# Kernel tuning notes

Measured on AMD Instinct MI355X. Metric: run time of the kernel, lower is better.

## Reference

```python
import jax, jax.numpy as jnp
import numpy as np

N, E = 10000, 160000
F_IN, H1, C1, C2 = 256, 8, 128, 128
SLOPE = 0.2  # PyG GATConv default negative_slope


def setup_inputs() -> dict:
    key = jax.random.key(0)
    ks = jax.random.split(key, 9)
    s = 0.05
    return {
        "x": jax.random.normal(ks[0], (N, F_IN), jnp.float32),
        "edge_index": jax.random.randint(ks[1], (2, E), 0, N),
        "W1": jax.random.normal(ks[2], (F_IN, H1 * C1), jnp.float32) * s,
        "a_src1": jax.random.normal(ks[3], (H1, C1), jnp.float32) * s,
        "a_dst1": jax.random.normal(ks[4], (H1, C1), jnp.float32) * s,
        "b1": jnp.zeros((H1 * C1,), jnp.float32),
        "W2": jax.random.normal(ks[5], (H1 * C1, C2), jnp.float32) * s,
        "a_src2": jax.random.normal(ks[6], (1, C2), jnp.float32) * s,
        "a_dst2": jax.random.normal(ks[7], (1, C2), jnp.float32) * s,
        "b2": jnp.zeros((C2,), jnp.float32),
    }


def gat_conv(x, src, dst, W, a_s, a_d, b, heads, out_ch, concat):
    n = x.shape[0]
    h = (x @ W).reshape(n, heads, out_ch)            # [N,H,C]
    s_src = jnp.einsum("nhc,hc->nh", h, a_s)         # [N,H]
    s_dst = jnp.einsum("nhc,hc->nh", h, a_d)
    e = jax.nn.leaky_relu(s_src[src] + s_dst[dst], SLOPE)   # [Etot,H]
    # segment softmax over incoming edges per destination (self-loops guarantee non-empty segments)
    m = jax.lax.stop_gradient(jax.ops.segment_max(e, dst, num_segments=n))
    p = jnp.exp(e - m[dst])
    denom = jax.ops.segment_sum(p, dst, num_segments=n)
    alpha = p / denom[dst]                            # [Etot,H]
    out = jax.ops.segment_sum(h[src] * alpha[:, :, None], dst, num_segments=n)  # [N,H,C]
    out = out.reshape(n, heads * out_ch) if concat else out.mean(axis=1)
    return out + b


def reference(x, edge_index, W1, a_src1, a_dst1, b1, W2, a_src2, a_dst2, b2):
    n = x.shape[0]
    loops = jnp.arange(n, dtype=edge_index.dtype)     # PyG add_self_loops=True
    src = jnp.concatenate([edge_index[0], loops])
    dst = jnp.concatenate([edge_index[1], loops])
    # dropout layers are identity at inference (training=False)
    h1 = jax.nn.elu(gat_conv(x, src, dst, W1, a_src1, a_dst1, b1, H1, C1, True))
    return gat_conv(h1, src, dst, W2, a_src2, a_dst2, b2, 1, C2, False)
```

## Files before the change

kernel.cpp:

```cpp
#include <hip/hip_runtime.h>
#include <math.h>

#define F_IN 256
#define H1 8
#define C1 128
#define HC1 1024
#define C2 128
#define SLOPE 0.2f

typedef unsigned short u16;
typedef __attribute__((ext_vector_type(8))) short bf16x8;
typedef __attribute__((ext_vector_type(4))) float f32x4;


__device__ __forceinline__ float lrelu(float v) { return v > 0.f ? v : SLOPE * v; }

__device__ __forceinline__ unsigned bf16_rne(float x) {
    unsigned u = __float_as_uint(x);
    u += 0x7fffu + ((u >> 16) & 1u);
    return u >> 16;
}

__device__ __forceinline__ void split2(float a, float b, unsigned& hi, unsigned& lo) {
    unsigned ha = bf16_rne(a), hb = bf16_rne(b);
    float fa = __uint_as_float(ha << 16), fb = __uint_as_float(hb << 16);
    hi = ha | (hb << 16);
    lo = bf16_rne(a - fa) | (bf16_rne(b - fb) << 16);
}

__device__ __forceinline__ void gload16(const u16* g, u16* l) {
    __builtin_amdgcn_global_load_lds(
        (const __attribute__((address_space(1))) unsigned*)g,
        (__attribute__((address_space(3))) unsigned*)l, 16, 0, 0);
}


__global__ void init_deg(int* deg, int n) {
    int i = blockIdx.x * blockDim.x + threadIdx.x;
    if (i < n) deg[i] = 1;
}

__global__ void hist_kernel(const int* __restrict__ dst, int* __restrict__ deg, int E) {
    int i = blockIdx.x * blockDim.x + threadIdx.x;
    if (i < E) atomicAdd(&deg[dst[i]], 1);
}

__global__ void scan_kernel(const int* __restrict__ deg, int* __restrict__ start,
                            int* __restrict__ cursor, int n) {
    __shared__ int buf[1024];
    int carry = 0;
    for (int base = 0; base < n; base += 1024) {
        int i = base + (int)threadIdx.x;
        int v = (i < n) ? deg[i] : 0;
        buf[threadIdx.x] = v;
        __syncthreads();
        for (int offd = 1; offd < 1024; offd <<= 1) {
            int tv = 0;
            if ((int)threadIdx.x >= offd) tv = buf[threadIdx.x - offd];
            __syncthreads();
            if ((int)threadIdx.x >= offd) buf[threadIdx.x] += tv;
            __syncthreads();
        }
        int incl = buf[threadIdx.x];
        if (i < n) { start[i] = carry + incl - v; cursor[i] = carry + incl - v; }
        carry += buf[1023];
        __syncthreads();
    }
    if (threadIdx.x == 0) start[n] = carry;
}

__global__ void scatter_kernel(const int* __restrict__ src, const int* __restrict__ dst,
                               int* __restrict__ cursor, int* __restrict__ ssorted,
                               unsigned char* __restrict__ rowloc,
                               int E, int N) {
    int i = blockIdx.x * blockDim.x + threadIdx.x;
    if (i < E) {
        int d = dst[i];
        int pos = atomicAdd(&cursor[d], 1);
        ssorted[pos] = src[i];
        rowloc[pos] = (unsigned char)(d & 15);
    } else if (i < E + N) {
        int d = i - E;
        int pos = atomicAdd(&cursor[d], 1);
        ssorted[pos] = d;
        rowloc[pos] = (unsigned char)(d & 15);
    }
}


__global__ void split_mat(const float* __restrict__ in, u16* __restrict__ hi,
                          u16* __restrict__ lo, int n) {
    int i = blockIdx.x * blockDim.x + threadIdx.x;
    if (i >= n) return;
    float v = in[i];
    unsigned h = bf16_rne(v);
    hi[i] = (u16)h;
    lo[i] = (u16)bf16_rne(v - __uint_as_float(h << 16));
}

__global__ void split_transpose(const float* __restrict__ in, u16* __restrict__ hi,
                                u16* __restrict__ lo, int R, int C) {
    int i = blockIdx.x * blockDim.x + threadIdx.x;
    if (i >= R * C) return;
    int r = i / C, c = i % C;
    float v = in[i];
    unsigned h = bf16_rne(v);
    hi[(size_t)c * R + r] = (u16)h;
    lo[(size_t)c * R + r] = (u16)bf16_rne(v - __uint_as_float(h << 16));
}


__global__ __launch_bounds__(256) void gemm_mfma(const u16* __restrict__ Ahi,
                                                 const u16* __restrict__ Alo,
                                                 const u16* __restrict__ Bhi,
                                                 const u16* __restrict__ Blo,
                                                 u16* __restrict__ Cbf,
                                                 int M, int N, int K) {
    __shared__ u16 lds[16384];
    const int t = threadIdx.x;
    const int rbase = blockIdx.y * 128;
    const int cbase = blockIdx.x * 128;

    const int lane = t & 63;
    const int R0 = (t >> 7) << 6;
    const int C0 = ((t >> 6) & 1) << 6;
    const int lrow = lane & 15;
    const int kq = lane >> 4;

    f32x4 acc[4][4] = {};

    for (int k0 = 0; k0 < K; k0 += 32) {
#pragma unroll
        for (int i = 0; i < 2; i++) {
            int c = t + (i << 8);
            int row = c >> 2;
            int kc = (c & 3) << 3;
            int ar = min(rbase + row, M - 1);
            int br = cbase + row;
            gload16(Ahi + (size_t)ar * K + k0 + kc, &lds[c * 8]);
            gload16(Alo + (size_t)ar * K + k0 + kc, &lds[4096 + c * 8]);
            gload16(Bhi + (size_t)br * K + k0 + kc, &lds[8192 + c * 8]);
            gload16(Blo + (size_t)br * K + k0 + kc, &lds[12288 + c * 8]);
        }
        __syncthreads();

        bf16x8 ah[4], al[4], bh[4], bl[4];
#pragma unroll
        for (int m = 0; m < 4; m++) {
            int off = (R0 + (m << 4) + lrow) * 32 + (kq << 3);
            ah[m] = *(const bf16x8*)&lds[off];
            al[m] = *(const bf16x8*)&lds[4096 + off];
        }
#pragma unroll
        for (int n = 0; n < 4; n++) {
            int off = (C0 + (n << 4) + lrow) * 32 + (kq << 3);
            bh[n] = *(const bf16x8*)&lds[8192 + off];
            bl[n] = *(const bf16x8*)&lds[12288 + off];
        }
#pragma unroll
        for (int m = 0; m < 4; m++)
#pragma unroll
            for (int n = 0; n < 4; n++) {
                acc[m][n] = __builtin_amdgcn_mfma_f32_16x16x32_bf16(ah[m], bh[n], acc[m][n], 0, 0, 0);
                acc[m][n] = __builtin_amdgcn_mfma_f32_16x16x32_bf16(ah[m], bl[n], acc[m][n], 0, 0, 0);
                acc[m][n] = __builtin_amdgcn_mfma_f32_16x16x32_bf16(al[m], bh[n], acc[m][n], 0, 0, 0);
            }
        __syncthreads();
    }

#pragma unroll
    for (int m = 0; m < 4; m++)
#pragma unroll
        for (int n = 0; n < 4; n++) {
            int col = cbase + C0 + (n << 4) + lrow;
#pragma unroll
            for (int r = 0; r < 4; r++) {
                int row = rbase + R0 + (m << 4) + kq * 4 + r;
                if (row < M) Cbf[(size_t)row * N + col] = (u16)bf16_rne(acc[m][n][r]);
            }
        }
}


__global__ __launch_bounds__(256) void gemm_mfma64(const u16* __restrict__ Ahi,
                                                   const u16* __restrict__ Alo,
                                                   const u16* __restrict__ Bhi,
                                                   const u16* __restrict__ Blo,
                                                   u16* __restrict__ Cbf,
                                                   int M, int N, int K) {
    __shared__ u16 lds[16384];
    const int t = threadIdx.x;
    const int rbase = blockIdx.y * 64;
    const int cbase = blockIdx.x * 64;

    const int lane = t & 63;
    const int w = t >> 6;
    const int R0 = (w >> 1) << 5;
    const int C0 = (w & 1) << 5;
    const int lrow = lane & 15;
    const int kq = lane >> 4;

    f32x4 acc[2][2] = {};

    for (int k0 = 0; k0 < K; k0 += 64) {
        {
            int row = (w << 4) + (lane >> 2);
            int kcc = (lane & 3) << 3;
            int ar = min(rbase + row, M - 1);
            int br = cbase + row;
            const size_t ga = (size_t)ar * K + k0 + kcc;
            const size_t gb = (size_t)br * K + k0 + kcc;
            const int ldo = row * 32 + kcc;
#pragma unroll
            for (int s2 = 0; s2 < 2; s2++) {
                gload16(Ahi + ga + s2 * 32, &lds[s2 * 2048 + ldo]);
                gload16(Alo + ga + s2 * 32, &lds[4096 + s2 * 2048 + ldo]);
                gload16(Bhi + gb + s2 * 32, &lds[8192 + s2 * 2048 + ldo]);
                gload16(Blo + gb + s2 * 32, &lds[12288 + s2 * 2048 + ldo]);
            }
        }
        __syncthreads();

#pragma unroll
        for (int s = 0; s < 2; s++) {
            bf16x8 ah[2], al[2], bh[2], bl[2];
#pragma unroll
            for (int m = 0; m < 2; m++) {
                int off = s * 2048 + (R0 + (m << 4) + lrow) * 32 + (kq << 3);
                ah[m] = *(const bf16x8*)&lds[off];
                al[m] = *(const bf16x8*)&lds[4096 + off];
            }
#pragma unroll
            for (int n = 0; n < 2; n++) {
                int off = s * 2048 + (C0 + (n << 4) + lrow) * 32 + (kq << 3);
                bh[n] = *(const bf16x8*)&lds[8192 + off];
                bl[n] = *(const bf16x8*)&lds[12288 + off];
            }
#pragma unroll
            for (int m = 0; m < 2; m++)
#pragma unroll
                for (int n = 0; n < 2; n++) {
                    acc[m][n] = __builtin_amdgcn_mfma_f32_16x16x32_bf16(ah[m], bh[n], acc[m][n], 0, 0, 0);
                    acc[m][n] = __builtin_amdgcn_mfma_f32_16x16x32_bf16(ah[m], bl[n], acc[m][n], 0, 0, 0);
                    acc[m][n] = __builtin_amdgcn_mfma_f32_16x16x32_bf16(al[m], bh[n], acc[m][n], 0, 0, 0);
                }
        }
        __syncthreads();
    }

#pragma unroll
    for (int m = 0; m < 2; m++)
#pragma unroll
        for (int n = 0; n < 2; n++) {
            int col = cbase + C0 + (n << 4) + lrow;
#pragma unroll
            for (int r = 0; r < 4; r++) {
                int row = rbase + R0 + (m << 4) + kq * 4 + r;
                if (row < M) Cbf[(size_t)row * N + col] = (u16)bf16_rne(acc[m][n][r]);
            }
        }
}


__global__ __launch_bounds__(256) void scores1_bf(const unsigned* __restrict__ hbf,
                                                  const float* __restrict__ a_s,
                                                  const float* __restrict__ a_d,
                                                  float* __restrict__ ssrc,
                                                  float* __restrict__ sdst, int N) {
    int wid = blockIdx.x * 4 + (threadIdx.x >> 6);
    if (wid >= N * H1) return;
    int lane = threadIdx.x & 63;
    int n = wid >> 3, hh = wid & 7;
    unsigned u = hbf[(size_t)n * 512 + hh * 64 + lane];
    float c0 = __uint_as_float(u << 16);
    float c1 = __uint_as_float(u & 0xffff0000u);
    const float* as = a_s + hh * C1;
    const float* ad = a_d + hh * C1;
    float vs = c0 * as[2 * lane] + c1 * as[2 * lane + 1];
    float vd = c0 * ad[2 * lane] + c1 * ad[2 * lane + 1];
    for (int off = 32; off; off >>= 1) {
        vs += __shfl_xor(vs, off);
        vd += __shfl_xor(vd, off);
    }
    if (lane == 0) { ssrc[wid] = vs; sdst[wid] = vd; }
}

__global__ __launch_bounds__(256) void scores2_bf(const unsigned* __restrict__ hbf,
                                                  const float* __restrict__ a_s,
                                                  const float* __restrict__ a_d,
                                                  float* __restrict__ ssrc,
                                                  float* __restrict__ sdst, int N) {
    int n = blockIdx.x * 4 + (threadIdx.x >> 6);
    if (n >= N) return;
    int lane = threadIdx.x & 63;
    unsigned u = hbf[(size_t)n * 64 + lane];
    float c0 = __uint_as_float(u << 16);
    float c1 = __uint_as_float(u & 0xffff0000u);
    float vs = c0 * a_s[2 * lane] + c1 * a_s[2 * lane + 1];
    float vd = c0 * a_d[2 * lane] + c1 * a_d[2 * lane + 1];
    for (int off = 32; off; off >>= 1) {
        vs += __shfl_xor(vs, off);
        vd += __shfl_xor(vd, off);
    }
    if (lane == 0) { ssrc[n] = vs; sdst[n] = vd; }
}


__global__ __launch_bounds__(256) void softmax_edges1(
    const float* __restrict__ ssrc, const float* __restrict__ sdst,
    const int* __restrict__ start, const int* __restrict__ ssorted,
    float* __restrict__ alphab, int N, int ET) {
    int lane = threadIdx.x & 63;
    int p = lane & 15, g = lane >> 4;
    int task = (blockIdx.x * 4 + (threadIdx.x >> 6)) * 4 + g;
    if (task >= N * H1) return;
    int d = task >> 3, hh = task & 7;
    int s0 = start[d], ne = start[d + 1] - s0;
    float sd = sdst[d * H1 + hh];
    int src0 = 0; float v0 = -1e30f;
    if (p < ne) { src0 = ssorted[s0 + p]; v0 = lrelu(ssrc[src0 * H1 + hh] + sd); }
    float m = v0;
    for (int e = p + 16; e < ne; e += 16)
        m = fmaxf(m, lrelu(ssrc[ssorted[s0 + e] * H1 + hh] + sd));
    for (int o = 8; o; o >>= 1) m = fmaxf(m, __shfl_xor(m, o));
    float p0 = (p < ne) ? __expf(v0 - m) : 0.f;
    float s = p0;
    for (int e = p + 16; e < ne; e += 16)
        s += __expf(lrelu(ssrc[ssorted[s0 + e] * H1 + hh] + sd) - m);
    for (int o = 8; o; o >>= 1) s += __shfl_xor(s, o);
    float inv = 1.f / s;
    float* ab = alphab + (size_t)hh * ET;
    if (p < ne) ab[s0 + p] = p0 * inv;
    for (int e = p + 16; e < ne; e += 16)
        ab[s0 + e] = __expf(lrelu(ssrc[ssorted[s0 + e] * H1 + hh] + sd) - m) * inv;
}


__global__ __launch_bounds__(256) void agg_mfma1(
    const u16* __restrict__ hbf,
    const float* __restrict__ alphab,
    const unsigned char* __restrict__ rowloc,
    const int* __restrict__ start,
    const int* __restrict__ ssorted,
    const float* __restrict__ bias,
    u16* __restrict__ outHi, u16* __restrict__ outLo,
    int N, int ET) {
    __shared__ unsigned A32[2][16 * 68];
    __shared__ int mOff[2][64];

    const int hh = blockIdx.x & 7;
    const int g = blockIdx.x >> 3;
    const int t = threadIdx.x;
    const int w = t >> 6;
    const int lane = t & 63;
    const int cl = lane & 15, q = lane >> 4;

    const int d0 = g * 16;
    const int e0 = start[d0], e1 = start[min(d0 + 16, N)];
    const float* ab = alphab + (size_t)hh * ET;

    const int lanebyte = hh * 256 + w * 64 + 4 * cl;
    const char* hbase = (const char*)hbf;

    const int nk = (e1 - e0 + 63) >> 6;

    auto fill = [&](int b, int kb) {
        unsigned* Az = &A32[b][(lane >> 2) * 68 + (lane & 3) * 16];
        uint4 z = {0u, 0u, 0u, 0u};
        *(uint4*)(Az) = z;
        *(uint4*)(Az + 4) = z;
        *(uint4*)(Az + 8) = z;
        *(uint4*)(Az + 12) = z;
        int pos = kb + lane;
        bool valid = pos < e1;
        int ps = valid ? pos : e0;
        float af = valid ? ab[ps] : 0.f;
        unsigned ahiu = bf16_rne(af);
        unsigned alou = bf16_rne(af - __uint_as_float(ahiu << 16));
        int rr = rowloc[ps];
        mOff[b][lane] = ssorted[ps] << 11;
        asm volatile("s_waitcnt lgkmcnt(0)" ::: "memory");
        A32[b][rr * 68 + lane] = ahiu | (alou << 16);
    };

    f32x4 acc0 = {}, acc1 = {};

    if (w == 0 && nk > 0) fill(0, e0);

    for (int i = 0; i < nk; ++i) {
        __syncthreads();
        const int b = i & 1;
        if (w == 0 && i + 1 < nk) fill(b ^ 1, e0 + (i + 1) * 64);

        const int mb = q * 8;
        int4 o0 = *(const int4*)&mOff[b][mb];
        int4 o1 = *(const int4*)&mOff[b][mb + 4];
        int4 o2 = *(const int4*)&mOff[b][32 + mb];
        int4 o3 = *(const int4*)&mOff[b][32 + mb + 4];
        int oo[16] = {o0.x, o0.y, o0.z, o0.w, o1.x, o1.y, o1.z, o1.w,
                      o2.x, o2.y, o2.z, o2.w, o3.x, o3.y, o3.z, o3.w};

        unsigned gld[16];
#pragma unroll
        for (int j = 0; j < 16; j++)
            gld[j] = *(const unsigned*)(hbase + (unsigned)(oo[j] + lanebyte));

        const unsigned* Ar = &A32[b][cl * 68 + mb];
        uint4 a0 = *(const uint4*)(Ar);
        uint4 a1 = *(const uint4*)(Ar + 4);
        uint4 a2 = *(const uint4*)(Ar + 32);
        uint4 a3 = *(const uint4*)(Ar + 36);
        unsigned aw[16] = {a0.x, a0.y, a0.z, a0.w, a1.x, a1.y, a1.z, a1.w,
                           a2.x, a2.y, a2.z, a2.w, a3.x, a3.y, a3.z, a3.w};

        union { unsigned u[4]; bf16x8 v; } ahi0, alo0, ahi1, alo1, b00, b10, b01, b11;
#pragma unroll
        for (int r = 0; r < 4; r++) {
            ahi0.u[r] = __builtin_amdgcn_perm(aw[2 * r + 1], aw[2 * r], 0x05040100u);
            alo0.u[r] = __builtin_amdgcn_perm(aw[2 * r + 1], aw[2 * r], 0x07060302u);
            ahi1.u[r] = __builtin_amdgcn_perm(aw[8 + 2 * r + 1], aw[8 + 2 * r], 0x05040100u);
            alo1.u[r] = __builtin_amdgcn_perm(aw[8 + 2 * r + 1], aw[8 + 2 * r], 0x07060302u);
            b00.u[r] = __builtin_amdgcn_perm(gld[2 * r + 1], gld[2 * r], 0x05040100u);
            b10.u[r] = __builtin_amdgcn_perm(gld[2 * r + 1], gld[2 * r], 0x07060302u);
            b01.u[r] = __builtin_amdgcn_perm(gld[8 + 2 * r + 1], gld[8 + 2 * r], 0x05040100u);
            b11.u[r] = __builtin_amdgcn_perm(gld[8 + 2 * r + 1], gld[8 + 2 * r], 0x07060302u);
        }

        acc0 = __builtin_amdgcn_mfma_f32_16x16x32_bf16(ahi0.v, b00.v, acc0, 0, 0, 0);
        acc0 = __builtin_amdgcn_mfma_f32_16x16x32_bf16(alo0.v, b00.v, acc0, 0, 0, 0);
        acc1 = __builtin_amdgcn_mfma_f32_16x16x32_bf16(ahi0.v, b10.v, acc1, 0, 0, 0);
        acc1 = __builtin_amdgcn_mfma_f32_16x16x32_bf16(alo0.v, b10.v, acc1, 0, 0, 0);
        acc0 = __builtin_amdgcn_mfma_f32_16x16x32_bf16(ahi1.v, b01.v, acc0, 0, 0, 0);
        acc0 = __builtin_amdgcn_mfma_f32_16x16x32_bf16(alo1.v, b01.v, acc0, 0, 0, 0);
        acc1 = __builtin_amdgcn_mfma_f32_16x16x32_bf16(ahi1.v, b11.v, acc1, 0, 0, 0);
        acc1 = __builtin_amdgcn_mfma_f32_16x16x32_bf16(alo1.v, b11.v, acc1, 0, 0, 0);
    }

    {
        int chbase = w * 32 + 2 * cl;
        float bv0 = bias[hh * C1 + chbase];
        float bv1 = bias[hh * C1 + chbase + 1];
#pragma unroll
        for (int r = 0; r < 4; r++) {
            int d = d0 + q * 4 + r;
            if (d >= N) continue;
            float v0 = acc0[r] + bv0;
            float v1 = acc1[r] + bv1;
            v0 = v0 > 0.f ? v0 : expm1f(v0);
            v1 = v1 > 0.f ? v1 : expm1f(v1);
            unsigned hi, lo;
            split2(v0, v1, hi, lo);
            size_t idx = (size_t)d * HC1 + hh * C1 + chbase;
            ((unsigned*)outHi)[idx >> 1] = hi;
            ((unsigned*)outLo)[idx >> 1] = lo;
        }
    }
}


template<int H, bool SPLITOUT>
__global__ __launch_bounds__(256) void agg_bf(const unsigned* __restrict__ hbf,
                                              const float* __restrict__ ssrc,
                                              const float* __restrict__ sdst,
                                              const int* __restrict__ start,
                                              const int* __restrict__ ssorted,
                                              const float* __restrict__ bias,
                                              float* __restrict__ out,
                                              unsigned* __restrict__ outHi,
                                              unsigned* __restrict__ outLo, int N) {
    int hh, grp;
    if (H == 8) { hh = blockIdx.x & 7; grp = blockIdx.x >> 3; }
    else        { hh = 0;              grp = blockIdx.x; }
    int wid = threadIdx.x >> 6, lane = threadIdx.x & 63;
    int d = grp * 4 + wid;
    if (d >= N) return;
    const int g = lane >> 4, p = lane & 15;
    int s0 = start[d];
    int ne = start[d + 1] - s0;
    float sd = sdst[d * H + hh];

    const unsigned* hlane = hbf + hh * 64 + p * 4;
    const int rowstride = H * 64;

    int src0 = 0; float v0 = -1e30f;
    if (lane < ne) { src0 = ssorted[s0 + lane]; v0 = lrelu(ssrc[src0 * H + hh] + sd); }
    float m = v0;
    for (int e = lane + 64; e < ne; e += 64)
        m = fmaxf(m, lrelu(ssrc[ssorted[s0 + e] * H + hh] + sd));
    for (int o = 32; o; o >>= 1) m = fmaxf(m, __shfl_xor(m, o));

    float p0 = (lane < ne) ? __expf(v0 - m) : 0.f;
    float ssum = p0;
    for (int e = lane + 64; e < ne; e += 64)
        ssum += __expf(lrelu(ssrc[ssorted[s0 + e] * H + hh] + sd) - m);
    for (int o = 32; o; o >>= 1) ssum += __shfl_xor(ssum, o);
    float inv = 1.f / ssum;

    float acc[8] = {};
    for (int base = 0; base < ne; base += 64) {
        int srcr; float al;
        if (base == 0) { srcr = src0; al = p0 * inv; }
        else {
            srcr = 0; al = 0.f;
            int e = base + lane;
            if (e < ne) {
                srcr = ssorted[s0 + e];
                al = __expf(lrelu(ssrc[srcr * H + hh] + sd) - m) * inv;
            }
        }
        int cnt = min(64, ne - base);
        for (int e2 = 0; e2 < cnt; e2 += 4) {
            float a = __shfl(al, e2 + g);
            int sr = __shfl(srcr, e2 + g);
            uint4 u = *(const uint4*)(hlane + (size_t)sr * rowstride);
            acc[0] += a * __uint_as_float(u.x << 16);
            acc[1] += a * __uint_as_float(u.x & 0xffff0000u);
            acc[2] += a * __uint_as_float(u.y << 16);
            acc[3] += a * __uint_as_float(u.y & 0xffff0000u);
            acc[4] += a * __uint_as_float(u.z << 16);
            acc[5] += a * __uint_as_float(u.z & 0xffff0000u);
            acc[6] += a * __uint_as_float(u.w << 16);
            acc[7] += a * __uint_as_float(u.w & 0xffff0000u);
        }
    }

#pragma unroll
    for (int i = 0; i < 8; i++) {
        acc[i] += __shfl_xor(acc[i], 16);
        acc[i] += __shfl_xor(acc[i], 32);
    }

    float r0 = g == 0 ? acc[0] : g == 1 ? acc[2] : g == 2 ? acc[4] : acc[6];
    float r1 = g == 0 ? acc[1] : g == 1 ? acc[3] : g == 2 ? acc[5] : acc[7];
    int j = 4 * p + g;
    float2 bv = ((const float2*)bias)[hh * 64 + j];
    r0 += bv.x; r1 += bv.y;
    size_t idx = (size_t)d * (H * 64) + hh * 64 + j;
    if (SPLITOUT) {
        r0 = r0 > 0.f ? r0 : expm1f(r0);
        r1 = r1 > 0.f ? r1 : expm1f(r1);
        unsigned hi, lo;
        split2(r0, r1, hi, lo);
        outHi[idx] = hi;
        outLo[idx] = lo;
    } else {
        ((float2*)out)[idx] = make_float2(r0, r1);
    }
}


extern "C" void kernel_launch(void* const* d_in, const int* in_sizes, int n_in,
                              void* d_out, int out_size, void* d_ws, size_t ws_size,
                              hipStream_t stream) {
    const float* x      = (const float*)d_in[0];
    const int*   ei     = (const int*)d_in[1];
    const float* W1     = (const float*)d_in[2];
    const float* a_src1 = (const float*)d_in[3];
    const float* a_dst1 = (const float*)d_in[4];
    const float* b1     = (const float*)d_in[5];
    const float* W2     = (const float*)d_in[6];
    const float* a_src2 = (const float*)d_in[7];
    const float* a_dst2 = (const float*)d_in[8];
    const float* b2     = (const float*)d_in[9];
    float* out = (float*)d_out;

    int E = in_sizes[1] / 2;
    int N = in_sizes[0] / F_IN;
    int ET = E + N;
    const int* esrc = ei;
    const int* edst = ei + E;

    char* ws = (char*)d_ws;
    size_t off = 0;
    auto alloc = [&](size_t bytes) -> char* {
        char* p = ws + off;
        off = (off + bytes + 255) & ~(size_t)255;
        return p;
    };
    u16* x_hi    = (u16*)alloc((size_t)N * F_IN * 2);
    u16* x_lo    = (u16*)alloc((size_t)N * F_IN * 2);
    u16* W1t_hi  = (u16*)alloc((size_t)F_IN * HC1 * 2);
    u16* W1t_lo  = (u16*)alloc((size_t)F_IN * HC1 * 2);
    u16* W2t_hi  = (u16*)alloc((size_t)HC1 * C2 * 2);
    u16* W2t_lo  = (u16*)alloc((size_t)HC1 * C2 * 2);
    u16* h1_bf   = (u16*)alloc((size_t)N * HC1 * 2);
    u16* h1a_hi  = (u16*)alloc((size_t)N * HC1 * 2);
    u16* h1a_lo  = (u16*)alloc((size_t)N * HC1 * 2);
    u16* h2_bf   = (u16*)alloc((size_t)N * C2 * 2);
    float* ss1   = (float*)alloc((size_t)N * H1 * 4);
    float* sd1   = (float*)alloc((size_t)N * H1 * 4);
    float* ss2   = (float*)alloc((size_t)N * 4);
    float* sd2   = (float*)alloc((size_t)N * 4);
    int* deg     = (int*)alloc((size_t)N * 4);
    int* startp  = (int*)alloc((size_t)(N + 1) * 4);
    int* cursor  = (int*)alloc((size_t)N * 4);
    int* ssorted = (int*)alloc((size_t)ET * 4);
    unsigned char* rowloc = (unsigned char*)alloc((size_t)ET);
    float* alpha1 = (float*)x_hi;

    init_deg<<<(N + 255) / 256, 256, 0, stream>>>(deg, N);
    hist_kernel<<<(E + 255) / 256, 256, 0, stream>>>(edst, deg, E);
    scan_kernel<<<1, 1024, 0, stream>>>(deg, startp, cursor, N);
    scatter_kernel<<<(E + N + 255) / 256, 256, 0, stream>>>(esrc, edst, cursor, ssorted, rowloc, E, N);

    split_mat<<<(N * F_IN + 255) / 256, 256, 0, stream>>>(x, x_hi, x_lo, N * F_IN);
    split_transpose<<<(F_IN * HC1 + 255) / 256, 256, 0, stream>>>(W1, W1t_hi, W1t_lo, F_IN, HC1);
    split_transpose<<<(HC1 * C2 + 255) / 256, 256, 0, stream>>>(W2, W2t_hi, W2t_lo, HC1, C2);

    gemm_mfma<<<dim3(HC1 / 128, (N + 127) / 128), 256, 0, stream>>>(
        x_hi, x_lo, W1t_hi, W1t_lo, h1_bf, N, HC1, F_IN);
    scores1_bf<<<(N * H1 + 3) / 4, 256, 0, stream>>>(
        (const unsigned*)h1_bf, a_src1, a_dst1, ss1, sd1, N);
    softmax_edges1<<<(N * H1 + 15) / 16, 256, 0, stream>>>(
        ss1, sd1, startp, ssorted, alpha1, N, ET);
    agg_mfma1<<<((N + 15) / 16) * H1, 256, 0, stream>>>(
        h1_bf, alpha1, rowloc, startp, ssorted, b1, h1a_hi, h1a_lo, N, ET);

    gemm_mfma64<<<dim3(C2 / 64, (N + 63) / 64), 256, 0, stream>>>(
        h1a_hi, h1a_lo, W2t_hi, W2t_lo, h2_bf, N, C2, HC1);
    scores2_bf<<<(N + 3) / 4, 256, 0, stream>>>(
        (const unsigned*)h2_bf, a_src2, a_dst2, ss2, sd2, N);
    agg_bf<1, false><<<(N + 3) / 4, 256, 0, stream>>>(
        (const unsigned*)h2_bf, ss2, sd2, startp, ssorted, b2,
        out, nullptr, nullptr, N);
}
```

Before: 248.4 us.

## Fuse layer-1 attention scores into GEMM epilogue and merge prep kernels

Computes the layer-1 source and destination attention scores inside the first GEMM epilogue from fp32 accumulators, using shuffle reductions and LDS. This removes the separate scores1 kernel and its re-read of h1. It also folds degree initialisation into the x split kernel, merges the two weight split-transposes into one launch, and replaces the barrier-heavy scan with a wave-shuffle scan. Scores now come from unrounded fp32 values rather than bf16, so numerics shift slightly.

```diff
diff --git a/kernel.cpp b/kernel.cpp
--- a/kernel.cpp
+++ b/kernel.cpp
@@ -35,11 +35,6 @@
 }
 
 
-__global__ void init_deg(int* deg, int n) {
-    int i = blockIdx.x * blockDim.x + threadIdx.x;
-    if (i < n) deg[i] = 1;
-}
-
 __global__ void hist_kernel(const int* __restrict__ dst, int* __restrict__ deg, int E) {
     int i = blockIdx.x * blockDim.x + threadIdx.x;
     if (i < E) atomicAdd(&deg[dst[i]], 1);
@@ -47,26 +42,41 @@
 
 __global__ void scan_kernel(const int* __restrict__ deg, int* __restrict__ start,
                             int* __restrict__ cursor, int n) {
-    __shared__ int buf[1024];
+    __shared__ int wsum[16];
+    __shared__ int wpre[16];
+    __shared__ int ctot;
+    const int tid = threadIdx.x;
+    const int lane = tid & 63, wv = tid >> 6;
     int carry = 0;
     for (int base = 0; base < n; base += 1024) {
-        int i = base + (int)threadIdx.x;
+        int i = base + tid;
         int v = (i < n) ? deg[i] : 0;
-        buf[threadIdx.x] = v;
-        __syncthreads();
-        for (int offd = 1; offd < 1024; offd <<= 1) {
-            int tv = 0;
-            if ((int)threadIdx.x >= offd) tv = buf[threadIdx.x - offd];
-            __syncthreads();
-            if ((int)threadIdx.x >= offd) buf[threadIdx.x] += tv;
-            __syncthreads();
-        }
-        int incl = buf[threadIdx.x];
-        if (i < n) { start[i] = carry + incl - v; cursor[i] = carry + incl - v; }
-        carry += buf[1023];
-        __syncthreads();
-    }
-    if (threadIdx.x == 0) start[n] = carry;
+        int x = v;
+#pragma unroll
+        for (int o = 1; o < 64; o <<= 1) {
+            int y = __shfl_up(x, o);
+            if (lane >= o) x += y;
+        }
+        if (lane == 63) wsum[wv] = x;
+        __syncthreads();
+        if (tid < 16) {
+            int s = wsum[tid];
+            int xx = s;
+#pragma unroll
+            for (int o = 1; o < 16; o <<= 1) {
+                int y = __shfl_up(xx, o);
+                if (tid >= o) xx += y;
+            }
+            wpre[tid] = xx - s;
+            if (tid == 15) ctot = xx;
+        }
+        __syncthreads();
+        int excl = carry + wpre[wv] + (x - v);
+        if (i < n) { start[i] = excl; cursor[i] = excl; }
+        carry += ctot;
+        __syncthreads();
+    }
+    if (tid == 0) start[n] = carry;
 }
 
 __global__ void scatter_kernel(const int* __restrict__ src, const int* __restrict__ dst,
@@ -88,9 +98,11 @@
 }
 
 
-__global__ void split_mat(const float* __restrict__ in, u16* __restrict__ hi,
-                          u16* __restrict__ lo, int n) {
+__global__ void split_mat_deg(const float* __restrict__ in, u16* __restrict__ hi,
+                              u16* __restrict__ lo, int n,
+                              int* __restrict__ deg, int nd) {
     int i = blockIdx.x * blockDim.x + threadIdx.x;
+    if (i < nd) deg[i] = 1;
     if (i >= n) return;
     float v = in[i];
     unsigned h = bf16_rne(v);
@@ -98,15 +110,27 @@
     lo[i] = (u16)bf16_rne(v - __uint_as_float(h << 16));
 }
 
-__global__ void split_transpose(const float* __restrict__ in, u16* __restrict__ hi,
-                                u16* __restrict__ lo, int R, int C) {
+__global__ void split_transpose2(const float* __restrict__ in1, u16* __restrict__ hi1,
+                                 u16* __restrict__ lo1, int R1, int Cc1,
+                                 const float* __restrict__ in2, u16* __restrict__ hi2,
+                                 u16* __restrict__ lo2, int R2, int Cc2) {
     int i = blockIdx.x * blockDim.x + threadIdx.x;
-    if (i >= R * C) return;
-    int r = i / C, c = i % C;
-    float v = in[i];
-    unsigned h = bf16_rne(v);
-    hi[(size_t)c * R + r] = (u16)h;
-    lo[(size_t)c * R + r] = (u16)bf16_rne(v - __uint_as_float(h << 16));
+    int n1 = R1 * Cc1;
+    if (i < n1) {
+        int r = i / Cc1, c = i % Cc1;
+        float v = in1[i];
+        unsigned h = bf16_rne(v);
+        hi1[(size_t)c * R1 + r] = (u16)h;
+        lo1[(size_t)c * R1 + r] = (u16)bf16_rne(v - __uint_as_float(h << 16));
+    } else {
+        int j = i - n1;
+        if (j >= R2 * Cc2) return;
+        int r = j / Cc2, c = j % Cc2;
+        float v = in2[j];
+        unsigned h = bf16_rne(v);
+        hi2[(size_t)c * R2 + r] = (u16)h;
+        lo2[(size_t)c * R2 + r] = (u16)bf16_rne(v - __uint_as_float(h << 16));
+    }
 }
 
 
@@ -115,7 +139,11 @@
                                                  const u16* __restrict__ Bhi,
                                                  const u16* __restrict__ Blo,
                                                  u16* __restrict__ Cbf,
-                                                 int M, int N, int K) {
+                                                 int M, int N, int K,
+                                                 const float* __restrict__ a_s,
+                                                 const float* __restrict__ a_d,
+                                                 float* __restrict__ ssrc,
+                                                 float* __restrict__ sdst) {
     __shared__ u16 lds[16384];
     const int t = threadIdx.x;
     const int rbase = blockIdx.y * 128;
@@ -179,6 +207,49 @@
                 if (row < M) Cbf[(size_t)row * N + col] = (u16)bf16_rne(acc[m][n][r]);
             }
         }
+
+    {
+        float* fl = (float*)lds;
+        const int head = blockIdx.x;
+        const int c01 = (t >> 6) & 1;
+        float asv[4], adv[4];
+#pragma unroll
+        for (int n = 0; n < 4; n++) {
+            int col = head * 128 + C0 + (n << 4) + lrow;
+            asv[n] = a_s[col];
+            adv[n] = a_d[col];
+        }
+#pragma unroll
+        for (int m = 0; m < 4; m++)
+#pragma unroll
+            for (int r = 0; r < 4; r++) {
+                float vs = 0.f, vd = 0.f;
+#pragma unroll
+                for (int n = 0; n < 4; n++) {
+                    float h = acc[m][n][r];
+                    vs += asv[n] * h;
+                    vd += adv[n] * h;
+                }
+#pragma unroll
+                for (int o = 1; o < 16; o <<= 1) {
+                    vs += __shfl_xor(vs, o);
+                    vd += __shfl_xor(vd, o);
+                }
+                if (lrow == 0) {
+                    int lr = R0 + (m << 4) + kq * 4 + r;
+                    fl[c01 * 128 + lr] = vs;
+                    fl[256 + c01 * 128 + lr] = vd;
+                }
+            }
+        __syncthreads();
+        if (t < 128) {
+            int row = rbase + t;
+            if (row < M) {
+                ssrc[row * H1 + head] = fl[t] + fl[128 + t];
+                sdst[row * H1 + head] = fl[256 + t] + fl[384 + t];
+            }
+        }
+    }
 }
 
 
@@ -261,29 +332,6 @@
         }
 }
 
-
-__global__ __launch_bounds__(256) void scores1_bf(const unsigned* __restrict__ hbf,
-                                                  const float* __restrict__ a_s,
-                                                  const float* __restrict__ a_d,
-                                                  float* __restrict__ ssrc,
-                                                  float* __restrict__ sdst, int N) {
-    int wid = blockIdx.x * 4 + (threadIdx.x >> 6);
-    if (wid >= N * H1) return;
-    int lane = threadIdx.x & 63;
-    int n = wid >> 3, hh = wid & 7;
-    unsigned u = hbf[(size_t)n * 512 + hh * 64 + lane];
-    float c0 = __uint_as_float(u << 16);
-    float c1 = __uint_as_float(u & 0xffff0000u);
-    const float* as = a_s + hh * C1;
-    const float* ad = a_d + hh * C1;
-    float vs = c0 * as[2 * lane] + c1 * as[2 * lane + 1];
-    float vd = c0 * ad[2 * lane] + c1 * ad[2 * lane + 1];
-    for (int off = 32; off; off >>= 1) {
-        vs += __shfl_xor(vs, off);
-        vd += __shfl_xor(vd, off);
-    }
-    if (lane == 0) { ssrc[wid] = vs; sdst[wid] = vd; }
-}
 
 __global__ __launch_bounds__(256) void scores2_bf(const unsigned* __restrict__ hbf,
                                                   const float* __restrict__ a_s,
@@ -598,19 +646,16 @@
     unsigned char* rowloc = (unsigned char*)alloc((size_t)ET);
     float* alpha1 = (float*)x_hi;
 
-    init_deg<<<(N + 255) / 256, 256, 0, stream>>>(deg, N);
+    split_mat_deg<<<(N * F_IN + 255) / 256, 256, 0, stream>>>(x, x_hi, x_lo, N * F_IN, deg, N);
     hist_kernel<<<(E + 255) / 256, 256, 0, stream>>>(edst, deg, E);
     scan_kernel<<<1, 1024, 0, stream>>>(deg, startp, cursor, N);
     scatter_kernel<<<(E + N + 255) / 256, 256, 0, stream>>>(esrc, edst, cursor, ssorted, rowloc, E, N);
 
-    split_mat<<<(N * F_IN + 255) / 256, 256, 0, stream>>>(x, x_hi, x_lo, N * F_IN);
-    split_transpose<<<(F_IN * HC1 + 255) / 256, 256, 0, stream>>>(W1, W1t_hi, W1t_lo, F_IN, HC1);
-    split_transpose<<<(HC1 * C2 + 255) / 256, 256, 0, stream>>>(W2, W2t_hi, W2t_lo, HC1, C2);
+    split_transpose2<<<(F_IN * HC1 + HC1 * C2 + 255) / 256, 256, 0, stream>>>(
+        W1, W1t_hi, W1t_lo, F_IN, HC1, W2, W2t_hi, W2t_lo, HC1, C2);
 
     gemm_mfma<<<dim3(HC1 / 128, (N + 127) / 128), 256, 0, stream>>>(
-        x_hi, x_lo, W1t_hi, W1t_lo, h1_bf, N, HC1, F_IN);
-    scores1_bf<<<(N * H1 + 3) / 4, 256, 0, stream>>>(
-        (const unsigned*)h1_bf, a_src1, a_dst1, ss1, sd1, N);
+        x_hi, x_lo, W1t_hi, W1t_lo, h1_bf, N, HC1, F_IN, a_src1, a_dst1, ss1, sd1);
     softmax_edges1<<<(N * H1 + 15) / 16, 256, 0, stream>>>(
         ss1, sd1, startp, ssorted, alpha1, N, ET);
     agg_mfma1<<<((N + 15) / 16) * H1, 256, 0, stream>>>(
```

New measurement: 229.4 us. 7.7% less time.
